# Kernel optimization log

Hardware: AMD Instinct MI355X
Metric: run time of the kernel (lower is better)

Reference implementation:

```python
import jax, jax.numpy as jnp
import numpy as np

N, F_IN, HID, E, G = 100000, 256, 256, 800000, 256


def setup_inputs() -> dict:
    key = jax.random.key(0)
    ks = jax.random.split(key, 10)
    x = jax.random.normal(ks[0], (N, F_IN), dtype=jnp.float32)
    edge_index = jax.random.randint(ks[1], (2, E), 0, N, dtype=jnp.int64)
    batch = jnp.sort(jax.random.randint(ks[2], (N,), 0, G, dtype=jnp.int64))
    s = 1.0 / np.sqrt(HID)
    W1 = jax.random.normal(ks[3], (F_IN, HID), dtype=jnp.float32) * s
    b1 = jnp.zeros((HID,), dtype=jnp.float32)
    W2 = jax.random.normal(ks[4], (HID, HID), dtype=jnp.float32) * s
    b2 = jnp.zeros((HID,), dtype=jnp.float32)
    Wc1 = jax.random.normal(ks[5], (HID, HID // 2), dtype=jnp.float32) * s
    bc1 = jnp.zeros((HID // 2,), dtype=jnp.float32)
    Wc2 = jax.random.normal(ks[6], (HID // 2, 2), dtype=jnp.float32) * s
    bc2 = jnp.zeros((2,), dtype=jnp.float32)
    return dict(x=x, edge_index=edge_index, batch=batch, num_graphs=G,
                W1=W1, b1=b1, W2=W2, b2=b2, Wc1=Wc1, bc1=bc1, Wc2=Wc2, bc2=bc2)


def _gcn_layer(h, src, dst, inv_sqrt_deg, W, b):
    # GCNConv: D^-1/2 (A + I) D^-1/2 (h W) + b
    hw = h @ W                                            # (N, H)
    coef = inv_sqrt_deg[src] * inv_sqrt_deg[dst]          # (E,)
    msgs = hw[src] * coef[:, None]                        # (E, H)
    agg = jax.ops.segment_sum(msgs, dst, num_segments=h.shape[0])
    self_loop = hw * (inv_sqrt_deg * inv_sqrt_deg)[:, None]
    return agg + self_loop + b


def reference(x, edge_index, batch, num_graphs, W1, b1, W2, b2, Wc1, bc1, Wc2, bc2):
    n = x.shape[0]
    src, dst = edge_index[0], edge_index[1]
    # degree with self-loops (symmetric normalization)
    deg = jax.ops.segment_sum(jnp.ones((src.shape[0],), jnp.float32), dst,
                              num_segments=n) + 1.0
    inv_sqrt_deg = jax.lax.rsqrt(deg)

    h = jax.nn.relu(_gcn_layer(x, src, dst, inv_sqrt_deg, W1, b1))
    node_emb = jax.nn.relu(_gcn_layer(h, src, dst, inv_sqrt_deg, W2, b2))

    # per-graph mean pooling (segment mean replacing the Python loop)
    sums = jax.ops.segment_sum(node_emb, batch, num_segments=num_graphs)
    counts = jax.ops.segment_sum(jnp.ones((n,), jnp.float32), batch,
                                 num_segments=num_graphs)
    graph_emb = sums / jnp.maximum(counts, 1.0)[:, None]

    # classifier MLP (dropout is identity in eval mode)
    hcls = jax.nn.relu(graph_emb @ Wc1 + bc1)
    logits = hcls @ Wc2 + bc2                             # (G, 2)
    return logits, node_emb
```

## Files before the change

### kernel.cpp

```cpp
#include <hip/hip_runtime.h>
#include <hip/hip_bf16.h>

#define HID 256
#define NGRAPH 256

typedef __bf16 bf16_t;
typedef __attribute__((ext_vector_type(8))) __bf16 bf16x8;
typedef __attribute__((ext_vector_type(4))) __bf16 bf16x4;
typedef __attribute__((ext_vector_type(4))) float f32x4;

__global__ void zero_int_kernel(int* __restrict__ p, int n) {
    int i = blockIdx.x * blockDim.x + threadIdx.x;
    if (i < n) p[i] = 0;
}

__global__ void count_deg_kernel(const int* __restrict__ ei, int E, int* __restrict__ deg) {
    int e = blockIdx.x * blockDim.x + threadIdx.x;
    if (e >= E) return;
    int dst = ei[E + e];
    atomicAdd(&deg[dst], 1);
}

#define SCHUNK 512

__global__ __launch_bounds__(256) void scan_pass1_kernel(
    const int* __restrict__ deg, int N, int* __restrict__ bsum) {
    __shared__ int red[256];
    int b = blockIdx.x, t = threadIdx.x;
    int i0 = b * SCHUNK + 2 * t;
    int v = 0;
    if (i0 < N) v += deg[i0];
    if (i0 + 1 < N) v += deg[i0 + 1];
    red[t] = v;
    __syncthreads();
    for (int s = 128; s > 0; s >>= 1) {
        if (t < s) red[t] += red[t + s];
        __syncthreads();
    }
    if (t == 0) bsum[b] = red[0];
}

__global__ __launch_bounds__(256) void scan_pass2_kernel(
    const int* __restrict__ bsum, int NB, int* __restrict__ boff) {
    __shared__ int s[256];
    int t = threadIdx.x;
    int v = (t < NB) ? bsum[t] : 0;
    s[t] = v;
    __syncthreads();
    for (int off = 1; off < 256; off <<= 1) {
        int x = s[t];
        if (t >= off) x += s[t - off];
        __syncthreads();
        s[t] = x;
        __syncthreads();
    }
    if (t < NB) boff[t] = s[t] - v;
}

__global__ __launch_bounds__(256) void scan_pass3_kernel(
    const int* __restrict__ deg, int N, const int* __restrict__ boff,
    int* __restrict__ rowptr, int* __restrict__ cursor, float* __restrict__ invd) {
    __shared__ int s[256];
    int b = blockIdx.x, t = threadIdx.x;
    int i0 = b * SCHUNK + 2 * t;
    int d0 = (i0 < N) ? deg[i0] : 0;
    int d1 = (i0 + 1 < N) ? deg[i0 + 1] : 0;
    int pair = d0 + d1;
    s[t] = pair;
    __syncthreads();
    for (int off = 1; off < 256; off <<= 1) {
        int x = s[t];
        if (t >= off) x += s[t - off];
        __syncthreads();
        s[t] = x;
        __syncthreads();
    }
    int excl = s[t] - pair + boff[b];
    if (i0 < N) {
        rowptr[i0] = excl;
        cursor[i0] = excl;
        invd[i0] = rsqrtf((float)d0 + 1.0f);
    }
    if (i0 + 1 < N) {
        int e1 = excl + d0;
        rowptr[i0 + 1] = e1;
        cursor[i0 + 1] = e1;
        invd[i0 + 1] = rsqrtf((float)d1 + 1.0f);
    }
}

__global__ void fill_csr_kernel(const int* __restrict__ ei, int E,
                                int* __restrict__ cursor, int* __restrict__ csr_src) {
    int e = blockIdx.x * blockDim.x + threadIdx.x;
    if (e >= E) return;
    int src = ei[e];
    int dst = ei[E + e];
    int pos = atomicAdd(&cursor[dst], 1);
    csr_src[pos] = src;
}

__global__ __launch_bounds__(256) void wsplit2_kernel(
    const float* __restrict__ W1, bf16_t* __restrict__ Wf1,
    const float* __restrict__ W2, bf16_t* __restrict__ Wf2) {
    int gi = blockIdx.x * 256 + threadIdx.x;
    const float* W = (gi < 65536) ? W1 : W2;
    bf16_t* Wf = (gi < 65536) ? Wf1 : Wf2;
    int idx = gi & 65535;
    float w = W[idx];
    int k = idx >> 8, n = idx & 255;
    int k0 = k >> 5, kg = (k >> 3) & 3, j = k & 7;
    int nt = n >> 4, m = n & 15;
    Wf[(size_t)(((k0 * 16 + nt) * 64) + kg * 16 + m) * 8 + j] = (bf16_t)w;
}

#define GBM 128

template <int INFP32>
__global__ __launch_bounds__(512, 4) void gemm_mfma_kernel(
    const void* __restrict__ Xv, const bf16_t* __restrict__ Wf,
    const float* __restrict__ rowscale, bf16_t* __restrict__ out, int Nrows) {
    __shared__ bf16_t Blds[32768];

    const int tid = threadIdx.x;
    const int wave = tid >> 6;
    const int lane = tid & 63;
    const int row0 = blockIdx.x * GBM;
    const int m = lane & 15;
    const int kg = lane >> 4;

    const int arow_raw = row0 + wave * 16 + m;
    const int arow = (arow_raw < Nrows) ? arow_raw : 0;

    f32x4 acc[16];
#pragma unroll
    for (int i = 0; i < 16; ++i) acc[i] = (f32x4){0.f, 0.f, 0.f, 0.f};

#pragma unroll
    for (int c = 0; c < 2; ++c) {
        float4 xa0, xb0, xa1, xb1, xa2, xb2, xa3, xb3;
        bf16x8 ah0, ah1, ah2, ah3;
        if (INFP32) {
            const float* xr = (const float*)Xv + (size_t)arow * 256 + c * 128 + kg * 8;
            xa0 = *(const float4*)&xr[0];   xb0 = *(const float4*)&xr[4];
            xa1 = *(const float4*)&xr[32];  xb1 = *(const float4*)&xr[36];
            xa2 = *(const float4*)&xr[64];  xb2 = *(const float4*)&xr[68];
            xa3 = *(const float4*)&xr[96];  xb3 = *(const float4*)&xr[100];
        } else {
            const bf16_t* xr = (const bf16_t*)Xv + (size_t)arow * 256 + c * 128 + kg * 8;
            ah0 = *(const bf16x8*)&xr[0];
            ah1 = *(const bf16x8*)&xr[32];
            ah2 = *(const bf16x8*)&xr[64];
            ah3 = *(const bf16x8*)&xr[96];
        }

        if (c) __syncthreads();
#pragma unroll
        for (int it = 0; it < 8; ++it)
            *(bf16x8*)&Blds[it * 4096 + tid * 8] =
                *(const bf16x8*)&Wf[c * 32768 + it * 4096 + tid * 8];
        __syncthreads();

#pragma unroll
        for (int k0c = 0; k0c < 4; ++k0c) {
            bf16x8 ah;
            if (INFP32) {
                float4 xa = (k0c == 0) ? xa0 : (k0c == 1) ? xa1 : (k0c == 2) ? xa2 : xa3;
                float4 xb = (k0c == 0) ? xb0 : (k0c == 1) ? xb1 : (k0c == 2) ? xb2 : xb3;
                float xf[8] = {xa.x, xa.y, xa.z, xa.w, xb.x, xb.y, xb.z, xb.w};
#pragma unroll
                for (int q = 0; q < 8; ++q) ah[q] = (bf16_t)xf[q];
            } else {
                ah = (k0c == 0) ? ah0 : (k0c == 1) ? ah1 : (k0c == 2) ? ah2 : ah3;
            }
#pragma unroll
            for (int nt = 0; nt < 16; ++nt) {
                bf16x8 bh = *(const bf16x8*)&Blds[(k0c * 16 + nt) * 512 + lane * 8];
                acc[nt] = __builtin_amdgcn_mfma_f32_16x16x32_bf16(ah, bh, acc[nt], 0, 0, 0);
            }
        }
    }

    const int rbase = row0 + wave * 16 + kg * 4;
#pragma unroll
    for (int j = 0; j < 4; ++j) {
        int r = rbase + j;
        if (r < Nrows) {
            float sc = rowscale[r];
#pragma unroll
            for (int nt = 0; nt < 16; ++nt)
                out[(size_t)r * 256 + nt * 16 + m] = (bf16_t)(acc[nt][j] * sc);
        }
    }
}

template <typename OutT>
__global__ __launch_bounds__(256) void gcn_aggregate_kernel(
    const bf16_t* __restrict__ hs, const int* __restrict__ rowptr,
    const int* __restrict__ deg, const int* __restrict__ csr_src,
    const float* __restrict__ inv_d, const float* __restrict__ bias,
    OutT* __restrict__ out, int N) {
    int gwid = (blockIdx.x * blockDim.x + threadIdx.x) >> 6;
    int lane = threadIdx.x & 63;
    int node = gwid * 2 + (lane >> 5);
    int hl = lane & 31;
    if (node >= N) return;
    int base = rowptr[node];
    int len = deg[node];
    int c = hl * 8;

    bf16x8 sv = *(const bf16x8*)&hs[(size_t)node * 256 + c];
    float a0[8], a1[8];
#pragma unroll
    for (int q = 0; q < 8; ++q) { a0[q] = (float)sv[q]; a1[q] = 0.f; }

    int i = 0;
    for (; i + 4 <= len; i += 4) {
        int s0 = csr_src[base + i];
        int s1 = csr_src[base + i + 1];
        int s2 = csr_src[base + i + 2];
        int s3 = csr_src[base + i + 3];
        bf16x8 v0 = *(const bf16x8*)&hs[(size_t)s0 * 256 + c];
        bf16x8 v1 = *(const bf16x8*)&hs[(size_t)s1 * 256 + c];
        bf16x8 v2 = *(const bf16x8*)&hs[(size_t)s2 * 256 + c];
        bf16x8 v3 = *(const bf16x8*)&hs[(size_t)s3 * 256 + c];
#pragma unroll
        for (int q = 0; q < 8; ++q) {
            a0[q] += (float)v0[q] + (float)v2[q];
            a1[q] += (float)v1[q] + (float)v3[q];
        }
    }
    for (; i < len; ++i) {
        int s = csr_src[base + i];
        bf16x8 v = *(const bf16x8*)&hs[(size_t)s * 256 + c];
#pragma unroll
        for (int q = 0; q < 8; ++q) a0[q] += (float)v[q];
    }

    float sc = inv_d[node];
    float4 bbA = *(const float4*)&bias[c];
    float4 bbB = *(const float4*)&bias[c + 4];
    float bb[8] = {bbA.x, bbA.y, bbA.z, bbA.w, bbB.x, bbB.y, bbB.z, bbB.w};
    float o[8];
#pragma unroll
    for (int q = 0; q < 8; ++q)
        o[q] = fmaxf(fmaf(a0[q] + a1[q], sc, bb[q]), 0.f);

    if constexpr (sizeof(OutT) == 2) {
        bf16x8 ov;
#pragma unroll
        for (int q = 0; q < 8; ++q) ov[q] = (bf16_t)o[q];
        *(bf16x8*)&out[(size_t)node * 256 + c] = ov;
    } else {
        float4 oA = {o[0], o[1], o[2], o[3]};
        float4 oB = {o[4], o[5], o[6], o[7]};
        *(float4*)&out[(size_t)node * 256 + c] = oA;
        *(float4*)&out[(size_t)node * 256 + c + 4] = oB;
    }
}

__global__ void graph_bounds_kernel(const int* __restrict__ batch, int N, int G,
                                    int* __restrict__ gstart) {
    int i = blockIdx.x * blockDim.x + threadIdx.x;
    if (i > N) return;
    int cur = (i < N) ? batch[i] : G;
    int prev = (i == 0) ? -1 : batch[i - 1];
    for (int g = prev + 1; g <= cur; ++g) gstart[g] = i;
}

__global__ __launch_bounds__(256) void pool_mean_kernel(
    const float* __restrict__ emb, const int* __restrict__ gstart,
    float* __restrict__ gemb) {
    __shared__ float red[4][64];
    int g = blockIdx.x;
    int col = blockIdx.y * 64 + (threadIdx.x & 63);
    int rg = threadIdx.x >> 6;
    int s = gstart[g], e = gstart[g + 1];
    float sum = 0.f;
    for (int n = s + rg; n < e; n += 4) sum += emb[(size_t)n * 256 + col];
    red[rg][threadIdx.x & 63] = sum;
    __syncthreads();
    if (rg == 0) {
        int l = threadIdx.x & 63;
        float t = (red[0][l] + red[1][l]) + (red[2][l] + red[3][l]);
        float cnt = fmaxf((float)(e - s), 1.0f);
        gemb[g * 256 + col] = t / cnt;
    }
}

__global__ __launch_bounds__(128) void cls1_kernel(
    const float* __restrict__ gemb, const float* __restrict__ Wc1,
    const float* __restrict__ bc1, float* __restrict__ hcls) {
    int g = blockIdx.x;
    int j = threadIdx.x;
    float sum = bc1[j];
    for (int k = 0; k < 256; ++k) sum = fmaf(gemb[g * 256 + k], Wc1[k * 128 + j], sum);
    hcls[g * 128 + j] = fmaxf(sum, 0.f);
}

__global__ void cls2_kernel(const float* __restrict__ hcls, const float* __restrict__ Wc2,
                            const float* __restrict__ bc2, float* __restrict__ logits, int G) {
    int idx = blockIdx.x * blockDim.x + threadIdx.x;
    if (idx >= G * 2) return;
    int g = idx >> 1, c = idx & 1;
    float sum = bc2[c];
    for (int k = 0; k < 128; ++k) sum = fmaf(hcls[g * 128 + k], Wc2[k * 2 + c], sum);
    logits[idx] = sum;
}

extern "C" void kernel_launch(void* const* d_in, const int* in_sizes, int n_in,
                              void* d_out, int out_size, void* d_ws, size_t ws_size,
                              hipStream_t stream) {
    const float* x   = (const float*)d_in[0];
    const int*   ei  = (const int*)d_in[1];
    const int*   batch = (const int*)d_in[2];
    const float* W1  = (const float*)d_in[4];
    const float* b1  = (const float*)d_in[5];
    const float* W2  = (const float*)d_in[6];
    const float* b2  = (const float*)d_in[7];
    const float* Wc1 = (const float*)d_in[8];
    const float* bc1 = (const float*)d_in[9];
    const float* Wc2 = (const float*)d_in[10];
    const float* bc2 = (const float*)d_in[11];

    const int N = in_sizes[0] / HID;
    const int E = in_sizes[1] / 2;
    const int G = NGRAPH;

    float* logits   = (float*)d_out;
    float* node_out = (float*)d_out + (size_t)G * 2;

    char* wsb = (char*)d_ws;
    size_t off = 0;
    auto alloc = [&](size_t bytes) -> void* {
        void* p = wsb + off;
        off += (bytes + 255) & ~(size_t)255;
        return p;
    };
    bf16_t* hs     = (bf16_t*)alloc((size_t)N * HID * 2);
    bf16_t* hb     = (bf16_t*)alloc((size_t)N * HID * 2);
    int*    rowptr = (int*)alloc((size_t)N * 4);
    int*    cursor = (int*)alloc((size_t)N * 4);
    int*    degi   = (int*)alloc((size_t)N * 4);
    int*    csr    = (int*)alloc((size_t)E * 4);
    float*  invd   = (float*)alloc((size_t)N * 4);
    int*    gstart = (int*)alloc((size_t)(G + 1) * 4);
    float*  gemb   = (float*)alloc((size_t)G * HID * 4);
    float*  hcls   = (float*)alloc((size_t)G * (HID / 2) * 4);
    int*    bsum   = (int*)alloc(256 * 4);
    int*    boff   = (int*)alloc(256 * 4);
    bf16_t* wf1    = (bf16_t*)alloc((size_t)HID * HID * 2);
    bf16_t* wf2    = (bf16_t*)alloc((size_t)HID * HID * 2);
    (void)ws_size; (void)n_in; (void)out_size;

    const int NB = (N + SCHUNK - 1) / SCHUNK;

    zero_int_kernel<<<(N + 255) / 256, 256, 0, stream>>>(degi, N);
    count_deg_kernel<<<(E + 255) / 256, 256, 0, stream>>>(ei, E, degi);
    scan_pass1_kernel<<<NB, 256, 0, stream>>>(degi, N, bsum);
    scan_pass2_kernel<<<1, 256, 0, stream>>>(bsum, NB, boff);
    scan_pass3_kernel<<<NB, 256, 0, stream>>>(degi, N, boff, rowptr, cursor, invd);
    fill_csr_kernel<<<(E + 255) / 256, 256, 0, stream>>>(ei, E, cursor, csr);
    wsplit2_kernel<<<2 * HID * HID / 256, 256, 0, stream>>>(W1, wf1, W2, wf2);

    const int GB = (N + GBM - 1) / GBM;
    const int AB = ((N + 1) / 2 * 64 + 255) / 256;

    gemm_mfma_kernel<1><<<GB, 512, 0, stream>>>(x, wf1, invd, hs, N);
    gcn_aggregate_kernel<bf16_t><<<AB, 256, 0, stream>>>(
        hs, rowptr, degi, csr, invd, b1, hb, N);

    gemm_mfma_kernel<0><<<GB, 512, 0, stream>>>(hb, wf2, invd, hs, N);
    gcn_aggregate_kernel<float><<<AB, 256, 0, stream>>>(
        hs, rowptr, degi, csr, invd, b2, node_out, N);

    graph_bounds_kernel<<<(N + 1 + 255) / 256, 256, 0, stream>>>(batch, N, G, gstart);
    pool_mean_kernel<<<dim3(G, 4), 256, 0, stream>>>(node_out, gstart, gemb);
    cls1_kernel<<<G, 128, 0, stream>>>(gemb, Wc1, bc1, hcls);
    cls2_kernel<<<(G * 2 + 255) / 256, 256, 0, stream>>>(hcls, Wc2, bc2, logits, G);
}
```

Measured before the change: 369.6 us.

## Merge small prep/classifier kernels and make GEMM persistent with resident weights

Combines the zero, weight-reformat, degree-count, graph-bounds and two classifier kernels into fewer launches to cut launch overhead. The GEMM becomes a persistent kernel with 256 blocks that load the full 256x256 bf16 weight into 128KB of LDS once, then loop over 64-row panels, with each wave covering 16 rows by half of the columns. This removes the repeated per-block weight staging and the mid-loop barrier, but lowers occupancy to at most 2 blocks per CU because of the LDS size, and relies on a fixed grid size.

```diff
diff --git a/kernel.cpp b/kernel.cpp
--- a/kernel.cpp
+++ b/kernel.cpp
@@ -9,16 +9,42 @@
 typedef __attribute__((ext_vector_type(4))) __bf16 bf16x4;
 typedef __attribute__((ext_vector_type(4))) float f32x4;
 
-__global__ void zero_int_kernel(int* __restrict__ p, int n) {
-    int i = blockIdx.x * blockDim.x + threadIdx.x;
-    if (i < n) p[i] = 0;
-}
-
-__global__ void count_deg_kernel(const int* __restrict__ ei, int E, int* __restrict__ deg) {
-    int e = blockIdx.x * blockDim.x + threadIdx.x;
-    if (e >= E) return;
-    int dst = ei[E + e];
-    atomicAdd(&deg[dst], 1);
+__global__ __launch_bounds__(256) void prep_kernel(
+    int* __restrict__ degi, int N, int ZB,
+    const float* __restrict__ W1, bf16_t* __restrict__ Wf1,
+    const float* __restrict__ W2, bf16_t* __restrict__ Wf2) {
+    int b = blockIdx.x;
+    if (b < ZB) {
+        int i = b * 256 + threadIdx.x;
+        if (i < N) degi[i] = 0;
+        return;
+    }
+    int gi = (b - ZB) * 256 + threadIdx.x;
+    const float* W = (gi < 65536) ? W1 : W2;
+    bf16_t* Wf = (gi < 65536) ? Wf1 : Wf2;
+    int idx = gi & 65535;
+    float w = W[idx];
+    int k = idx >> 8, n = idx & 255;
+    int k0 = k >> 5, kg = (k >> 3) & 3, j = k & 7;
+    int nt = n >> 4, m = n & 15;
+    Wf[(size_t)(((k0 * 16 + nt) * 64) + kg * 16 + m) * 8 + j] = (bf16_t)w;
+}
+
+__global__ void count_bounds_kernel(const int* __restrict__ ei, int E, int CB,
+                                    int* __restrict__ deg,
+                                    const int* __restrict__ batch, int N, int G,
+                                    int* __restrict__ gstart) {
+    int b = blockIdx.x;
+    if (b < CB) {
+        int e = b * 256 + threadIdx.x;
+        if (e < E) atomicAdd(&deg[ei[E + e]], 1);
+        return;
+    }
+    int i = (b - CB) * 256 + threadIdx.x;
+    if (i > N) return;
+    int cur = (i < N) ? batch[i] : G;
+    int prev = (i == 0) ? -1 : batch[i - 1];
+    for (int g = prev + 1; g <= cur; ++g) gstart[g] = i;
 }
 
 #define SCHUNK 512
@@ -99,96 +125,79 @@
     csr_src[pos] = src;
 }
 
-__global__ __launch_bounds__(256) void wsplit2_kernel(
-    const float* __restrict__ W1, bf16_t* __restrict__ Wf1,
-    const float* __restrict__ W2, bf16_t* __restrict__ Wf2) {
-    int gi = blockIdx.x * 256 + threadIdx.x;
-    const float* W = (gi < 65536) ? W1 : W2;
-    bf16_t* Wf = (gi < 65536) ? Wf1 : Wf2;
-    int idx = gi & 65535;
-    float w = W[idx];
-    int k = idx >> 8, n = idx & 255;
-    int k0 = k >> 5, kg = (k >> 3) & 3, j = k & 7;
-    int nt = n >> 4, m = n & 15;
-    Wf[(size_t)(((k0 * 16 + nt) * 64) + kg * 16 + m) * 8 + j] = (bf16_t)w;
-}
-
-#define GBM 128
+#define GBM 64
 
 template <int INFP32>
-__global__ __launch_bounds__(512, 4) void gemm_mfma_kernel(
+__global__ __launch_bounds__(512, 2) void gemm_mfma_kernel(
     const void* __restrict__ Xv, const bf16_t* __restrict__ Wf,
-    const float* __restrict__ rowscale, bf16_t* __restrict__ out, int Nrows) {
-    __shared__ bf16_t Blds[32768];
+    const float* __restrict__ rowscale, bf16_t* __restrict__ out,
+    int Nrows, int npanels) {
+    __shared__ bf16_t Blds[65536];
 
     const int tid = threadIdx.x;
     const int wave = tid >> 6;
     const int lane = tid & 63;
-    const int row0 = blockIdx.x * GBM;
     const int m = lane & 15;
     const int kg = lane >> 4;
-
-    const int arow_raw = row0 + wave * 16 + m;
-    const int arow = (arow_raw < Nrows) ? arow_raw : 0;
-
-    f32x4 acc[16];
-#pragma unroll
-    for (int i = 0; i < 16; ++i) acc[i] = (f32x4){0.f, 0.f, 0.f, 0.f};
-
-#pragma unroll
-    for (int c = 0; c < 2; ++c) {
-        float4 xa0, xb0, xa1, xb1, xa2, xb2, xa3, xb3;
-        bf16x8 ah0, ah1, ah2, ah3;
+    const int wr = (wave & 3) * 16 + m;
+    const int ntb = (wave >> 2) * 8;
+
+#pragma unroll
+    for (int it = 0; it < 16; ++it)
+        *(bf16x8*)&Blds[it * 4096 + tid * 8] =
+            *(const bf16x8*)&Wf[it * 4096 + tid * 8];
+    __syncthreads();
+
+    for (int p = blockIdx.x; p < npanels; p += gridDim.x) {
+        const int row0 = p * GBM;
+        int arow = row0 + wr;
+        if (arow >= Nrows) arow = 0;
+
+        bf16x8 af[8];
         if (INFP32) {
-            const float* xr = (const float*)Xv + (size_t)arow * 256 + c * 128 + kg * 8;
-            xa0 = *(const float4*)&xr[0];   xb0 = *(const float4*)&xr[4];
-            xa1 = *(const float4*)&xr[32];  xb1 = *(const float4*)&xr[36];
-            xa2 = *(const float4*)&xr[64];  xb2 = *(const float4*)&xr[68];
-            xa3 = *(const float4*)&xr[96];  xb3 = *(const float4*)&xr[100];
+            const float* xr = (const float*)Xv + (size_t)arow * 256 + kg * 8;
+            float4 xa[8], xb[8];
+#pragma unroll
+            for (int k0 = 0; k0 < 8; ++k0) {
+                xa[k0] = *(const float4*)&xr[k0 * 32];
+                xb[k0] = *(const float4*)&xr[k0 * 32 + 4];
+            }
+#pragma unroll
+            for (int k0 = 0; k0 < 8; ++k0) {
+                float xf[8] = {xa[k0].x, xa[k0].y, xa[k0].z, xa[k0].w,
+                               xb[k0].x, xb[k0].y, xb[k0].z, xb[k0].w};
+#pragma unroll
+                for (int q = 0; q < 8; ++q) af[k0][q] = (bf16_t)xf[q];
+            }
         } else {
-            const bf16_t* xr = (const bf16_t*)Xv + (size_t)arow * 256 + c * 128 + kg * 8;
-            ah0 = *(const bf16x8*)&xr[0];
-            ah1 = *(const bf16x8*)&xr[32];
-            ah2 = *(const bf16x8*)&xr[64];
-            ah3 = *(const bf16x8*)&xr[96];
+            const bf16_t* xr = (const bf16_t*)Xv + (size_t)arow * 256 + kg * 8;
+#pragma unroll
+            for (int k0 = 0; k0 < 8; ++k0)
+                af[k0] = *(const bf16x8*)&xr[k0 * 32];
         }
 
-        if (c) __syncthreads();
-#pragma unroll
-        for (int it = 0; it < 8; ++it)
-            *(bf16x8*)&Blds[it * 4096 + tid * 8] =
-                *(const bf16x8*)&Wf[c * 32768 + it * 4096 + tid * 8];
-        __syncthreads();
-
-#pragma unroll
-        for (int k0c = 0; k0c < 4; ++k0c) {
-            bf16x8 ah;
-            if (INFP32) {
-                float4 xa = (k0c == 0) ? xa0 : (k0c == 1) ? xa1 : (k0c == 2) ? xa2 : xa3;
-                float4 xb = (k0c == 0) ? xb0 : (k0c == 1) ? xb1 : (k0c == 2) ? xb2 : xb3;
-                float xf[8] = {xa.x, xa.y, xa.z, xa.w, xb.x, xb.y, xb.z, xb.w};
-#pragma unroll
-                for (int q = 0; q < 8; ++q) ah[q] = (bf16_t)xf[q];
-            } else {
-                ah = (k0c == 0) ? ah0 : (k0c == 1) ? ah1 : (k0c == 2) ? ah2 : ah3;
+        f32x4 acc[8];
+#pragma unroll
+        for (int i = 0; i < 8; ++i) acc[i] = (f32x4){0.f, 0.f, 0.f, 0.f};
+
+#pragma unroll
+        for (int k0 = 0; k0 < 8; ++k0)
+#pragma unroll
+            for (int nt = 0; nt < 8; ++nt) {
+                bf16x8 bh = *(const bf16x8*)&Blds[(size_t)(k0 * 16 + ntb + nt) * 512 + lane * 8];
+                acc[nt] = __builtin_amdgcn_mfma_f32_16x16x32_bf16(af[k0], bh, acc[nt], 0, 0, 0);
             }
-#pragma unroll
-            for (int nt = 0; nt < 16; ++nt) {
-                bf16x8 bh = *(const bf16x8*)&Blds[(k0c * 16 + nt) * 512 + lane * 8];
-                acc[nt] = __builtin_amdgcn_mfma_f32_16x16x32_bf16(ah, bh, acc[nt], 0, 0, 0);
+
+        const int rbase = row0 + (wave & 3) * 16 + kg * 4;
+#pragma unroll
+        for (int j = 0; j < 4; ++j) {
+            int r = rbase + j;
+            if (r < Nrows) {
+                float sc = rowscale[r];
+#pragma unroll
+                for (int nt = 0; nt < 8; ++nt)
+                    out[(size_t)r * 256 + (ntb + nt) * 16 + m] = (bf16_t)(acc[nt][j] * sc);
             }
-        }
-    }
-
-    const int rbase = row0 + wave * 16 + kg * 4;
-#pragma unroll
-    for (int j = 0; j < 4; ++j) {
-        int r = rbase + j;
-        if (r < Nrows) {
-            float sc = rowscale[r];
-#pragma unroll
-            for (int nt = 0; nt < 16; ++nt)
-                out[(size_t)r * 256 + nt * 16 + m] = (bf16_t)(acc[nt][j] * sc);
         }
     }
 }
@@ -258,15 +267,6 @@
     }
 }
 
-__global__ void graph_bounds_kernel(const int* __restrict__ batch, int N, int G,
-                                    int* __restrict__ gstart) {
-    int i = blockIdx.x * blockDim.x + threadIdx.x;
-    if (i > N) return;
-    int cur = (i < N) ? batch[i] : G;
-    int prev = (i == 0) ? -1 : batch[i - 1];
-    for (int g = prev + 1; g <= cur; ++g) gstart[g] = i;
-}
-
 __global__ __launch_bounds__(256) void pool_mean_kernel(
     const float* __restrict__ emb, const int* __restrict__ gstart,
     float* __restrict__ gemb) {
@@ -287,24 +287,21 @@
     }
 }
 
-__global__ __launch_bounds__(128) void cls1_kernel(
+__global__ __launch_bounds__(128) void cls_kernel(
     const float* __restrict__ gemb, const float* __restrict__ Wc1,
-    const float* __restrict__ bc1, float* __restrict__ hcls) {
-    int g = blockIdx.x;
-    int j = threadIdx.x;
+    const float* __restrict__ bc1, const float* __restrict__ Wc2,
+    const float* __restrict__ bc2, float* __restrict__ logits) {
+    __shared__ float hl[128];
+    int g = blockIdx.x, j = threadIdx.x;
     float sum = bc1[j];
     for (int k = 0; k < 256; ++k) sum = fmaf(gemb[g * 256 + k], Wc1[k * 128 + j], sum);
-    hcls[g * 128 + j] = fmaxf(sum, 0.f);
-}
-
-__global__ void cls2_kernel(const float* __restrict__ hcls, const float* __restrict__ Wc2,
-                            const float* __restrict__ bc2, float* __restrict__ logits, int G) {
-    int idx = blockIdx.x * blockDim.x + threadIdx.x;
-    if (idx >= G * 2) return;
-    int g = idx >> 1, c = idx & 1;
-    float sum = bc2[c];
-    for (int k = 0; k < 128; ++k) sum = fmaf(hcls[g * 128 + k], Wc2[k * 2 + c], sum);
-    logits[idx] = sum;
+    hl[j] = fmaxf(sum, 0.f);
+    __syncthreads();
+    if (j < 2) {
+        float s = bc2[j];
+        for (int k = 0; k < 128; ++k) s = fmaf(hl[k], Wc2[k * 2 + j], s);
+        logits[g * 2 + j] = s;
+    }
 }
 
 extern "C" void kernel_launch(void* const* d_in, const int* in_sizes, int n_in,
@@ -345,7 +342,6 @@
     float*  invd   = (float*)alloc((size_t)N * 4);
     int*    gstart = (int*)alloc((size_t)(G + 1) * 4);
     float*  gemb   = (float*)alloc((size_t)G * HID * 4);
-    float*  hcls   = (float*)alloc((size_t)G * (HID / 2) * 4);
     int*    bsum   = (int*)alloc(256 * 4);
     int*    boff   = (int*)alloc(256 * 4);
     bf16_t* wf1    = (bf16_t*)alloc((size_t)HID * HID * 2);
@@ -353,28 +349,28 @@
     (void)ws_size; (void)n_in; (void)out_size;
 
     const int NB = (N + SCHUNK - 1) / SCHUNK;
-
-    zero_int_kernel<<<(N + 255) / 256, 256, 0, stream>>>(degi, N);
-    count_deg_kernel<<<(E + 255) / 256, 256, 0, stream>>>(ei, E, degi);
+    const int ZB = (N + 255) / 256;
+    const int CB = (E + 255) / 256;
+    const int BB = (N + 1 + 255) / 256;
+
+    prep_kernel<<<ZB + 2 * HID * HID / 256, 256, 0, stream>>>(degi, N, ZB, W1, wf1, W2, wf2);
+    count_bounds_kernel<<<CB + BB, 256, 0, stream>>>(ei, E, CB, degi, batch, N, G, gstart);
     scan_pass1_kernel<<<NB, 256, 0, stream>>>(degi, N, bsum);
     scan_pass2_kernel<<<1, 256, 0, stream>>>(bsum, NB, boff);
     scan_pass3_kernel<<<NB, 256, 0, stream>>>(degi, N, boff, rowptr, cursor, invd);
     fill_csr_kernel<<<(E + 255) / 256, 256, 0, stream>>>(ei, E, cursor, csr);
-    wsplit2_kernel<<<2 * HID * HID / 256, 256, 0, stream>>>(W1, wf1, W2, wf2);
-
-    const int GB = (N + GBM - 1) / GBM;
+
+    const int NP = (N + GBM - 1) / GBM;
     const int AB = ((N + 1) / 2 * 64 + 255) / 256;
 
-    gemm_mfma_kernel<1><<<GB, 512, 0, stream>>>(x, wf1, invd, hs, N);
+    gemm_mfma_kernel<1><<<256, 512, 0, stream>>>(x, wf1, invd, hs, N, NP);
     gcn_aggregate_kernel<bf16_t><<<AB, 256, 0, stream>>>(
         hs, rowptr, degi, csr, invd, b1, hb, N);
 
-    gemm_mfma_kernel<0><<<GB, 512, 0, stream>>>(hb, wf2, invd, hs, N);
+    gemm_mfma_kernel<0><<<256, 512, 0, stream>>>(hb, wf2, invd, hs, N, NP);
     gcn_aggregate_kernel<float><<<AB, 256, 0, stream>>>(
         hs, rowptr, degi, csr, invd, b2, node_out, N);
 
-    graph_bounds_kernel<<<(N + 1 + 255) / 256, 256, 0, stream>>>(batch, N, G, gstart);
     pool_mean_kernel<<<dim3(G, 4), 256, 0, stream>>>(node_out, gstart, gemb);
-    cls1_kernel<<<G, 128, 0, stream>>>(gemb, Wc1, bc1, hcls);
-    cls2_kernel<<<(G * 2 + 255) / 256, 256, 0, stream>>>(hcls, Wc2, bc2, logits, G);
-}
+    cls_kernel<<<G, 128, 0, stream>>>(gemb, Wc1, bc1, Wc2, bc2, logits);
+}
```

After: 477.8 us. +29.3%, slower.
